# Optimization experiments

Hardware: AMD Instinct MI355X
Metric: run time of the kernel (lower is better)

Reference implementation:

```python
import jax, jax.numpy as jnp
import numpy as np

BATCH, N_SITES, BOND, PHYS = 4096, 1024, 32, 2
NOISE = 0.001  # keep trace of long product positive so log() is finite in fp32


def setup_inputs() -> dict:
    key = jax.random.key(0)
    k1, k2 = jax.random.split(key)
    s = jax.random.normal(k1, (BATCH, N_SITES), dtype=jnp.float32)
    # MPS tensor A[p] = I + small noise (same shapes/math as the module's param;
    # identity offset keeps the 1024-matrix product numerically benign)
    A = jnp.eye(BOND, dtype=jnp.float32)[None, :, :] + NOISE * jax.random.normal(
        k2, (PHYS, BOND, BOND), dtype=jnp.float32)
    return {"s": s, "A": A}


def reference(s, A):
    # s: [B, N] float; A: [phys, D, D]
    s_idx = (s > 0).astype(jnp.int32)               # phys_dim == 2 path: [B, N]
    B = s.shape[0]
    D = A.shape[-1]
    init = jnp.broadcast_to(jnp.eye(D, dtype=A.dtype), (B, D, D))

    def contract_site(carry, idx):
        # gather per-sample site matrix [B, D, D], batched matmul
        return jnp.matmul(carry, A[idx]), None

    final_prod, _ = jax.lax.scan(contract_site, init, s_idx.T)  # scan over N sites
    val = jnp.trace(final_prod, axis1=1, axis2=2)               # [B]
    return jnp.log(val)
```

## Files before the change

### kernel.cpp

```cpp
#include <hip/hip_runtime.h>
#include <hip/hip_bf16.h>


#define BATCH   4096
#define N_SITES 1024
#define NKEYS   256
#define NSTEP   128

typedef __attribute__((ext_vector_type(8)))  short    short8;
typedef __attribute__((ext_vector_type(16))) float    f32x16;
typedef __attribute__((ext_vector_type(4)))  unsigned uint4v;

static __device__ __forceinline__ unsigned short f32_to_bf16(float f) {
  unsigned u = __builtin_bit_cast(unsigned, f);
  const unsigned rounding = 0x7FFFu + ((u >> 16) & 1u);
  return (unsigned short)((u + rounding) >> 16);
}

static __device__ __forceinline__ unsigned cvt_pk_bf16(float lo, float hi) {
  unsigned r;
  asm("v_cvt_pk_bf16_f32 %0, %1, %2" : "=v"(r) : "v"(lo), "v"(hi));
  return r;
}

__global__ __launch_bounds__(256) void build_table_k(const float* __restrict__ A,
                                                     unsigned short* __restrict__ table) {
  __shared__ float As[2][32][32];
  __shared__ float M[2][32][32];
  const int key = blockIdx.x;
  const int t   = threadIdx.x;

  for (int i = t; i < 2 * 32 * 32; i += 256) ((float*)As)[i] = A[i];

  const int row = t >> 3;
  const int col = (t & 7) << 2;
  __syncthreads();

  {
    const int b0 = key & 1;
    const float4 v = *reinterpret_cast<const float4*>(&As[b0][row][col]);
    *reinterpret_cast<float4*>(&M[0][row][col]) = v;
  }
  __syncthreads();

  int cur = 0;
  for (int i = 1; i < 8; ++i) {
    const int bi = (key >> i) & 1;
    float a0 = 0.f, a1 = 0.f, a2 = 0.f, a3 = 0.f;
    for (int k = 0; k < 32; ++k) {
      const float m  = M[cur][row][k];
      const float4 v = *reinterpret_cast<const float4*>(&As[bi][k][col]);
      a0 += m * v.x; a1 += m * v.y; a2 += m * v.z; a3 += m * v.w;
    }
    M[cur ^ 1][row][col + 0] = a0;
    M[cur ^ 1][row][col + 1] = a1;
    M[cur ^ 1][row][col + 2] = a2;
    M[cur ^ 1][row][col + 3] = a3;
    __syncthreads();
    cur ^= 1;
  }

  const int c    = t >> 7;
  const int l    = (t >> 1) & 63;
  const int e4   = (t & 1) << 2;
  const int rowm = l & 31;
  const int hi   = l >> 5;

  unsigned long long packed = 0;
  for (int e = 0; e < 4; ++e) {
    const int k = c * 16 + (hi << 3) + e4 + e;
    const unsigned short us = f32_to_bf16(M[cur][k][rowm]);
    packed |= (unsigned long long)us << (16 * e);
  }
  *reinterpret_cast<unsigned long long*>(table + (size_t)key * 1024 + c * 512 + l * 8 + e4) = packed;
}

__global__ __launch_bounds__(256) void mps_chain_k(const float* __restrict__ s,
                                                   const unsigned short* __restrict__ table,
                                                   float* __restrict__ out) {
  const int wave = threadIdx.x >> 6;
  const int lane = threadIdx.x & 63;
  const int b    = blockIdx.x * 4 + wave;

  __shared__ unsigned char keys[4][NSTEP + 8];

  const float*  srow = s + (size_t)b * N_SITES;
  const float4* s4   = reinterpret_cast<const float4*>(srow) + lane * 4;
  unsigned k0 = 0, k1 = 0;
#pragma unroll
  for (int q = 0; q < 4; ++q) {
    const float4 v = s4[q];
    const unsigned m = (v.x > 0.f ? 1u : 0u) | (v.y > 0.f ? 2u : 0u) |
                       (v.z > 0.f ? 4u : 0u) | (v.w > 0.f ? 8u : 0u);
    if (q < 2) k0 |= m << (q * 4);
    else       k1 |= m << ((q - 2) * 4);
  }
  keys[wave][2 * lane]     = (unsigned char)k0;
  keys[wave][2 * lane + 1] = (unsigned char)k1;
  if (lane < 8) keys[wave][NSTEP + lane] = 0;
  __syncthreads();

  const int col = lane & 31;
  const int hi  = lane >> 5;

  f32x16 acc;
#pragma unroll
  for (int r = 0; r < 16; ++r) {
    const int rr = (r & 3) + 8 * (r >> 2) + 4 * hi;
    acc[r] = (rr == col) ? 1.f : 0.f;
  }

  const unsigned char* kw = keys[wave];
  const unsigned long long laneoff = (unsigned long long)lane * 8;

  unsigned kA = kw[0], kB = kw[1];
  unsigned kC = kw[2];
  const unsigned short* e0 = table + (size_t)kA * 1024;
  const unsigned short* e1 = table + (size_t)kB * 1024;
  uint4v c0 = *reinterpret_cast<const uint4v*>(e0 + laneoff);
  uint4v c1 = *reinterpret_cast<const uint4v*>(e0 + 512 + laneoff);
  uint4v n0 = *reinterpret_cast<const uint4v*>(e1 + laneoff);
  uint4v n1 = *reinterpret_cast<const uint4v*>(e1 + 512 + laneoff);

#pragma unroll 4
  for (int j = 0; j < NSTEP; ++j) {
    const unsigned short* ef = table + (size_t)kC * 1024;
    const uint4v f0 = *reinterpret_cast<const uint4v*>(ef + laneoff);
    const uint4v f1 = *reinterpret_cast<const uint4v*>(ef + 512 + laneoff);
    kC = kw[j + 3];

    unsigned pk[8];
#pragma unroll
    for (int i = 0; i < 8; ++i) pk[i] = cvt_pk_bf16(acc[2 * i], acc[2 * i + 1]);
    const auto s0 = __builtin_amdgcn_permlane32_swap((int)pk[0], (int)pk[2], false, false);
    const auto s1 = __builtin_amdgcn_permlane32_swap((int)pk[1], (int)pk[3], false, false);
    const auto s2 = __builtin_amdgcn_permlane32_swap((int)pk[4], (int)pk[6], false, false);
    const auto s3 = __builtin_amdgcn_permlane32_swap((int)pk[5], (int)pk[7], false, false);

    union { unsigned u[4]; short8 v; } B1, B2;
    B1.u[0] = (unsigned)s0[0]; B1.u[1] = (unsigned)s1[0];
    B1.u[2] = (unsigned)s0[1]; B1.u[3] = (unsigned)s1[1];
    B2.u[0] = (unsigned)s2[0]; B2.u[1] = (unsigned)s3[0];
    B2.u[2] = (unsigned)s2[1]; B2.u[3] = (unsigned)s3[1];

    union { uint4v q; short8 v; } ua0, ua1;
    ua0.q = c0; ua1.q = c1;

    f32x16 z;
#pragma unroll
    for (int r = 0; r < 16; ++r) z[r] = 0.f;

    f32x16 t1 = __builtin_amdgcn_mfma_f32_32x32x16_bf16(ua0.v, B1.v, z, 0, 0, 0);
    acc = __builtin_amdgcn_mfma_f32_32x32x16_bf16(ua1.v, B2.v, t1, 0, 0, 0);

    c0 = n0; c1 = n1; n0 = f0; n1 = f1;
  }

  float diag = 0.f;
#pragma unroll
  for (int r = 0; r < 16; ++r) {
    const int rr = (r & 3) + 8 * (r >> 2) + 4 * hi;
    if (rr == col) diag = acc[r];
  }
  const bool has = (((col >> 2) & 1) == hi);
  diag = has ? diag : 0.f;
#pragma unroll
  for (int off = 32; off > 0; off >>= 1) diag += __shfl_down(diag, off, 64);
  if (lane == 0) out[b] = logf(diag);
}

extern "C" void kernel_launch(void* const* d_in, const int* in_sizes, int n_in,
                              void* d_out, int out_size, void* d_ws, size_t ws_size,
                              hipStream_t stream) {
  const float* s = (const float*)d_in[0];
  const float* A = (const float*)d_in[1];
  float* out = (float*)d_out;
  unsigned short* table = (unsigned short*)d_ws;

  build_table_k<<<NKEYS, 256, 0, stream>>>(A, table);
  mps_chain_k<<<BATCH / 4, 256, 0, stream>>>(s, table, out);
}
```

Baseline: 114.9 us.

## Split each sample's matrix chain across two waves and combine via trace of product

Each batch sample now uses two waves, each multiplying half of the 128 key-matrices, which halves the serial MFMA dependency chain per wave. The second wave writes its product to shared memory in skewed layout, and the first wave computes trace(P1*P2) as an elementwise dot product. This doubles the wave count and adds a block-wide sync plus shared-memory exchange, trading more parallelism against extra launch blocks and LDS traffic.

```diff
diff --git a/kernel.cpp b/kernel.cpp
--- a/kernel.cpp
+++ b/kernel.cpp
@@ -5,7 +5,7 @@
 #define BATCH   4096
 #define N_SITES 1024
 #define NKEYS   256
-#define NSTEP   128
+#define NSTEP_H 64
 
 typedef __attribute__((ext_vector_type(8)))  short    short8;
 typedef __attribute__((ext_vector_type(16))) float    f32x16;
@@ -78,26 +78,26 @@
 __global__ __launch_bounds__(256) void mps_chain_k(const float* __restrict__ s,
                                                    const unsigned short* __restrict__ table,
                                                    float* __restrict__ out) {
-  const int wave = threadIdx.x >> 6;
-  const int lane = threadIdx.x & 63;
-  const int b    = blockIdx.x * 4 + wave;
+  const int t    = threadIdx.x;
+  const int pair = t >> 7;
+  const int wv   = (t >> 6) & 1;
+  const int lane = t & 63;
+  const int b    = blockIdx.x * 2 + pair;
 
-  __shared__ unsigned char keys[4][NSTEP + 8];
+  __shared__ unsigned char keys[2][128 + 8];
+  __shared__ float Ht[2][1024];
 
-  const float*  srow = s + (size_t)b * N_SITES;
-  const float4* s4   = reinterpret_cast<const float4*>(srow) + lane * 4;
-  unsigned k0 = 0, k1 = 0;
-#pragma unroll
-  for (int q = 0; q < 4; ++q) {
-    const float4 v = s4[q];
-    const unsigned m = (v.x > 0.f ? 1u : 0u) | (v.y > 0.f ? 2u : 0u) |
-                       (v.z > 0.f ? 4u : 0u) | (v.w > 0.f ? 8u : 0u);
-    if (q < 2) k0 |= m << (q * 4);
-    else       k1 |= m << ((q - 2) * 4);
-  }
-  keys[wave][2 * lane]     = (unsigned char)k0;
-  keys[wave][2 * lane + 1] = (unsigned char)k1;
-  if (lane < 8) keys[wave][NSTEP + lane] = 0;
+  const int kidx = wv * 64 + lane;
+  const float4* s4 = reinterpret_cast<const float4*>(s) + (size_t)b * 256 + kidx * 2;
+  const float4 va = s4[0];
+  const float4 vb = s4[1];
+  const unsigned key =
+      (va.x > 0.f ? 1u : 0u)  | (va.y > 0.f ? 2u : 0u)  |
+      (va.z > 0.f ? 4u : 0u)  | (va.w > 0.f ? 8u : 0u)  |
+      (vb.x > 0.f ? 16u : 0u) | (vb.y > 0.f ? 32u : 0u) |
+      (vb.z > 0.f ? 64u : 0u) | (vb.w > 0.f ? 128u : 0u);
+  keys[pair][kidx] = (unsigned char)key;
+  if (t < 16) keys[t >> 3][128 + (t & 7)] = 0;
   __syncthreads();
 
   const int col = lane & 31;
@@ -110,7 +110,7 @@
     acc[r] = (rr == col) ? 1.f : 0.f;
   }
 
-  const unsigned char* kw = keys[wave];
+  const unsigned char* kw = keys[pair] + wv * NSTEP_H;
   const unsigned long long laneoff = (unsigned long long)lane * 8;
 
   unsigned kA = kw[0], kB = kw[1];
@@ -123,7 +123,7 @@
   uint4v n1 = *reinterpret_cast<const uint4v*>(e1 + 512 + laneoff);
 
 #pragma unroll 4
-  for (int j = 0; j < NSTEP; ++j) {
+  for (int j = 0; j < NSTEP_H; ++j) {
     const unsigned short* ef = table + (size_t)kC * 1024;
     const uint4v f0 = *reinterpret_cast<const uint4v*>(ef + laneoff);
     const uint4v f1 = *reinterpret_cast<const uint4v*>(ef + 512 + laneoff);
@@ -156,17 +156,25 @@
     c0 = n0; c1 = n1; n0 = f0; n1 = f1;
   }
 
-  float diag = 0.f;
+  if (wv == 1) {
 #pragma unroll
-  for (int r = 0; r < 16; ++r) {
-    const int rr = (r & 3) + 8 * (r >> 2) + 4 * hi;
-    if (rr == col) diag = acc[r];
+    for (int r = 0; r < 16; ++r) {
+      const int a = (r & 3) + 8 * (r >> 2) + 4 * hi;
+      Ht[pair][col * 32 + ((a + col) & 31)] = acc[r];
+    }
   }
-  const bool has = (((col >> 2) & 1) == hi);
-  diag = has ? diag : 0.f;
+  __syncthreads();
+  if (wv == 0) {
+    float dot = 0.f;
 #pragma unroll
-  for (int off = 32; off > 0; off >>= 1) diag += __shfl_down(diag, off, 64);
-  if (lane == 0) out[b] = logf(diag);
+    for (int r = 0; r < 16; ++r) {
+      const int k = (r & 3) + 8 * (r >> 2) + 4 * hi;
+      dot += acc[r] * Ht[pair][k * 32 + ((col + k) & 31)];
+    }
+#pragma unroll
+    for (int off = 32; off > 0; off >>= 1) dot += __shfl_down(dot, off, 64);
+    if (lane == 0) out[b] = logf(dot);
+  }
 }
 
 extern "C" void kernel_launch(void* const* d_in, const int* in_sizes, int n_in,
@@ -178,5 +186,5 @@
   unsigned short* table = (unsigned short*)d_ws;
 
   build_table_k<<<NKEYS, 256, 0, stream>>>(A, table);
-  mps_chain_k<<<BATCH / 4, 256, 0, stream>>>(s, table, out);
+  mps_chain_k<<<BATCH / 2, 256, 0, stream>>>(s, table, out);
 }
```

Result: no change. 114.3 us (-0.5%).
